# Performance work log

Measured on AMD Instinct MI355X. Metric: run time of the kernel, lower is better.

Reference implementation:

```python
import jax, jax.numpy as jnp
import numpy as np


def setup_inputs() -> dict:
    key = jax.random.key(0)
    k1, k2 = jax.random.split(key)
    B, L, W = 256, 64, 512
    # refractive indices in [1, 3], thicknesses in [50, 250] nm, wavelengths 400-800 nm
    n_layers = 1.0 + 2.0 * jax.random.uniform(k1, (B, L), dtype=jnp.float32)
    d_layers = 50.0 + 200.0 * jax.random.uniform(k2, (B, L), dtype=jnp.float32)
    wavelengths = jnp.linspace(400.0, 800.0, W, dtype=jnp.float32)
    return {"n_layers": n_layers, "d_layers": d_layers, "wavelengths": wavelengths}


def reference(n_layers, d_layers, wavelengths):
    # n_layers: (B, L) real -> complex64; d_layers: (B, L); wavelengths: (W,)
    n = n_layers.astype(jnp.complex64)[:, :, None]          # (B, L, 1)
    d = d_layers[:, :, None]                                 # (B, L, 1) real
    lam = wavelengths[None, None, :]                         # (1, 1, W)

    n_i = n[:, 1:-1, :]                                      # (B, Li, 1) active films
    d_i = d[:, 1:-1, :]
    k0 = 2.0 * jnp.pi / lam                                  # (1, 1, W)
    phi = n_i * d_i * k0                                     # (B, Li, W) complex

    cos_phi = jnp.cos(phi)
    sin_phi = jnp.sin(phi)
    m11 = cos_phi
    m12 = (-1j) * sin_phi / (n_i + 1e-8)
    m21 = (-1j) * n_i * sin_phi
    m22 = cos_phi
    # (B, Li, W, 2, 2) characteristic matrices
    M_all = jnp.stack([jnp.stack([m11, m12], axis=-1),
                       jnp.stack([m21, m22], axis=-1)], axis=-2)
    M_all = jnp.moveaxis(M_all, 1, 0)                        # (Li, B, W, 2, 2)

    B_, W_ = phi.shape[0], phi.shape[2]
    M0 = jnp.broadcast_to(jnp.eye(2, dtype=jnp.complex64), (B_, W_, 2, 2))

    def body(carry, M_layer):
        # left-to-right product: M_total = M_total @ M_layer
        return jnp.einsum('bwij,bwjk->bwik', carry, M_layer), None

    M_total, _ = jax.lax.scan(body, M0, M_all)               # (B, W, 2, 2)

    n_in = n[:, 0, 0][:, None]                               # (B, 1) incident medium
    n_sub = n[:, -1, 0][:, None]                              # (B, 1) substrate
    # EH_in = M_total @ [1, n_sub]^T
    E_in = M_total[:, :, 0, 0] + M_total[:, :, 0, 1] * n_sub  # (B, W)
    H_in = M_total[:, :, 1, 0] + M_total[:, :, 1, 1] * n_sub
    Y_in = H_in / (E_in + 1e-9)
    r = (n_in - Y_in) / (n_in + Y_in)
    R = jnp.abs(r) ** 2                                       # (B, W) real
    return R.astype(jnp.float32)
```

## Files before the change

### kernel.cpp

```cpp
#include <hip/hip_runtime.h>
#include <math.h>


#define TMM_B 256
#define TMM_L 64
#define TMM_W 512

__global__ __launch_bounds__(256) void tmm_kernel(
    const float* __restrict__ n_layers,
    const float* __restrict__ d_layers,
    const float* __restrict__ wavelengths,
    float* __restrict__ out)
{
    __shared__ float s_n[TMM_L];
    __shared__ float s_nd[TMM_L];
    __shared__ float s_invn[TMM_L];

    const int b     = blockIdx.x >> 1;
    const int wbase = (blockIdx.x & 1) << 8;
    const int tid   = threadIdx.x;

    if (tid < TMM_L) {
        float n = n_layers[b * TMM_L + tid];
        float d = d_layers[b * TMM_L + tid];
        s_n[tid]    = n;
        s_nd[tid]   = n * d;
        s_invn[tid] = __frcp_rn(n + 1e-8f);
    }
    __syncthreads();

    const int w       = wbase + tid;
    const float lam   = wavelengths[w];
    const float ilam  = __frcp_rn(lam);

    float A = 1.0f, Bi = 0.0f, Ci = 0.0f, D = 1.0f;

    #pragma unroll
    for (int l = 1; l <= TMM_L - 2; ++l) {
        const float n    = s_n[l];
        const float rev  = s_nd[l] * ilam;
        const float sp   = __builtin_amdgcn_sinf(rev);
        const float cp   = __builtin_amdgcn_cosf(rev);
        const float bco  = -sp * s_invn[l];
        const float cco  = -n * sp;
        const float A2 = A  * cp - Bi * cco;
        const float B2 = A  * bco + Bi * cp;
        const float C2 = Ci * cp + D  * cco;
        const float D2 = D  * cp - Ci * bco;
        A = A2; Bi = B2; Ci = C2; D = D2;
    }

    const float n_in  = s_n[0];
    const float n_sub = s_n[TMM_L - 1];

    const float E_re = A + 1e-9f;
    const float E_im = Bi * n_sub;
    const float H_re = D * n_sub;
    const float H_im = Ci;

    const float num_re = n_in * E_re - H_re;
    const float num_im = n_in * E_im - H_im;
    const float den_re = n_in * E_re + H_re;
    const float den_im = n_in * E_im + H_im;

    const float R = (num_re * num_re + num_im * num_im) /
                    (den_re * den_re + den_im * den_im);

    out[b * TMM_W + w] = R;
}

extern "C" void kernel_launch(void* const* d_in, const int* in_sizes, int n_in,
                              void* d_out, int out_size, void* d_ws, size_t ws_size,
                              hipStream_t stream) {
    const float* n_layers    = (const float*)d_in[0];
    const float* d_layers    = (const float*)d_in[1];
    const float* wavelengths = (const float*)d_in[2];
    float* out = (float*)d_out;

    dim3 grid(TMM_B * 2);
    dim3 block(256);
    tmm_kernel<<<grid, block, 0, stream>>>(n_layers, d_layers, wavelengths, out);
}
```

Baseline: 59.87 us.

## Split layer-product chain across four wavefronts and combine partial matrices

The serial 62-layer transfer-matrix chain for each wavelength is split into four segments of 16, 16, 16 and 14 layers. Each segment is computed by a separate wavefront. The partial 2x2 matrices are staged in shared memory, and one wavefront multiplies them in order before computing reflectance. The grid grows fourfold, which shortens the dependent chain and raises occupancy. In exchange the kernel adds a barrier, shared-memory traffic and a tail step where only one of four wavefronts works.

```diff
diff --git a/kernel.cpp b/kernel.cpp
--- a/kernel.cpp
+++ b/kernel.cpp
@@ -15,58 +15,98 @@
     __shared__ float s_n[TMM_L];
     __shared__ float s_nd[TMM_L];
     __shared__ float s_invn[TMM_L];
+    __shared__ float s_pA[4][64];
+    __shared__ float s_pB[4][64];
+    __shared__ float s_pC[4][64];
+    __shared__ float s_pD[4][64];
 
-    const int b     = blockIdx.x >> 1;
-    const int wbase = (blockIdx.x & 1) << 8;
-    const int tid   = threadIdx.x;
+    const int b    = blockIdx.x >> 3;
+    const int wgrp = blockIdx.x & 7;
+    const int tid  = threadIdx.x;
+    const int wl   = tid & 63;
+    const int g    = tid >> 6;
 
     if (tid < TMM_L) {
-        float n = n_layers[b * TMM_L + tid];
-        float d = d_layers[b * TMM_L + tid];
+        const float n = n_layers[b * TMM_L + tid];
+        const float d = d_layers[b * TMM_L + tid];
         s_n[tid]    = n;
         s_nd[tid]   = n * d;
         s_invn[tid] = __frcp_rn(n + 1e-8f);
     }
     __syncthreads();
 
-    const int w       = wbase + tid;
-    const float lam   = wavelengths[w];
-    const float ilam  = __frcp_rn(lam);
+    const int w       = (wgrp << 6) | wl;
+    const float ilam  = __frcp_rn(wavelengths[w]);
 
     float A = 1.0f, Bi = 0.0f, Ci = 0.0f, D = 1.0f;
 
-    #pragma unroll
-    for (int l = 1; l <= TMM_L - 2; ++l) {
-        const float n    = s_n[l];
-        const float rev  = s_nd[l] * ilam;
-        const float sp   = __builtin_amdgcn_sinf(rev);
-        const float cp   = __builtin_amdgcn_cosf(rev);
-        const float bco  = -sp * s_invn[l];
-        const float cco  = -n * sp;
-        const float A2 = A  * cp - Bi * cco;
-        const float B2 = A  * bco + Bi * cp;
-        const float C2 = Ci * cp + D  * cco;
-        const float D2 = D  * cp - Ci * bco;
-        A = A2; Bi = B2; Ci = C2; D = D2;
+#define TMM_STEP(l) do {                                            \
+        const float n_   = s_n[(l)];             \
+        const float rev  = s_nd[(l)] * ilam;                        \
+        const float sp   = __builtin_amdgcn_sinf(rev);   \
+        const float cp   = __builtin_amdgcn_cosf(rev);   \
+        const float bco  = -sp * s_invn[(l)];                       \
+        const float cco  = -n_ * sp;                                \
+        const float A2 = A  * cp  - Bi * cco;                       \
+        const float B2 = A  * bco + Bi * cp;                        \
+        const float C2 = Ci * cp  + D  * cco;                       \
+        const float D2 = D  * cp  - Ci * bco;                       \
+        A = A2; Bi = B2; Ci = C2; D = D2;                           \
+    } while (0)
+
+    if (g == 3) {
+        #pragma unroll
+        for (int i = 0; i < 14; ++i) TMM_STEP(49 + i);
+    } else {
+        const int base = 1 + g * 16;
+        #pragma unroll
+        for (int i = 0; i < 16; ++i) TMM_STEP(base + i);
     }
+#undef TMM_STEP
 
-    const float n_in  = s_n[0];
-    const float n_sub = s_n[TMM_L - 1];
+    s_pA[g][wl] = A;
+    s_pB[g][wl] = Bi;
+    s_pC[g][wl] = Ci;
+    s_pD[g][wl] = D;
+    __syncthreads();
 
-    const float E_re = A + 1e-9f;
-    const float E_im = Bi * n_sub;
-    const float H_re = D * n_sub;
-    const float H_im = Ci;
+    if (tid < 64) {
+        const float a0 = s_pA[0][wl], b0 = s_pB[0][wl], c0 = s_pC[0][wl], d0 = s_pD[0][wl];
+        const float a1 = s_pA[1][wl], b1 = s_pB[1][wl], c1 = s_pC[1][wl], d1 = s_pD[1][wl];
+        const float a2 = s_pA[2][wl], b2 = s_pB[2][wl], c2 = s_pC[2][wl], d2 = s_pD[2][wl];
+        const float a3 = s_pA[3][wl], b3 = s_pB[3][wl], c3 = s_pC[3][wl], d3 = s_pD[3][wl];
 
-    const float num_re = n_in * E_re - H_re;
-    const float num_im = n_in * E_im - H_im;
-    const float den_re = n_in * E_re + H_re;
-    const float den_im = n_in * E_im + H_im;
+        const float qa = a0*a1 - b0*c1;
+        const float qb = a0*b1 + b0*d1;
+        const float qc = c0*a1 + d0*c1;
+        const float qd = d0*d1 - c0*b1;
+        const float ra = a2*a3 - b2*c3;
+        const float rb = a2*b3 + b2*d3;
+        const float rc = c2*a3 + d2*c3;
+        const float rd = d2*d3 - c2*b3;
+        const float MA = qa*ra - qb*rc;
+        const float MB = qa*rb + qb*rd;
+        const float MC = qc*ra + qd*rc;
+        const float MD = qd*rd - qc*rb;
 
-    const float R = (num_re * num_re + num_im * num_im) /
-                    (den_re * den_re + den_im * den_im);
+        const float n_in  = s_n[0];
+        const float n_sub = s_n[TMM_L - 1];
 
-    out[b * TMM_W + w] = R;
+        const float E_re = MA + 1e-9f;
+        const float E_im = MB * n_sub;
+        const float H_re = MD * n_sub;
+        const float H_im = MC;
+
+        const float num_re = n_in * E_re - H_re;
+        const float num_im = n_in * E_im - H_im;
+        const float den_re = n_in * E_re + H_re;
+        const float den_im = n_in * E_im + H_im;
+
+        const float R = (num_re * num_re + num_im * num_im) /
+                        (den_re * den_re + den_im * den_im);
+
+        out[b * TMM_W + w] = R;
+    }
 }
 
 extern "C" void kernel_launch(void* const* d_in, const int* in_sizes, int n_in,
@@ -77,7 +117,7 @@
     const float* wavelengths = (const float*)d_in[2];
     float* out = (float*)d_out;
 
-    dim3 grid(TMM_B * 2);
+    dim3 grid(TMM_B * 8);
     dim3 block(256);
     tmm_kernel<<<grid, block, 0, stream>>>(n_layers, d_layers, wavelengths, out);
 }
```

Measured after the change: 60.08 us. About the same (+0.4%).
